# Optimization experiments

Hardware: AMD Instinct MI355X
Metric: run time of the kernel (lower is better)

## Reference

```python
import jax, jax.numpy as jnp
import numpy as np

N = 100000  # nodes (in_features)
D = 32      # out_features
E = 1600000 # edges


def setup_inputs() -> dict:
    key = jax.random.key(0)
    k1, k2, k3, k4, k5 = jax.random.split(key, 5)
    edge_row = jax.random.randint(k1, (E,), 0, N, dtype=jnp.int64)
    edge_col = jax.random.randint(k2, (E,), 0, N, dtype=jnp.int64)
    edge_val = jax.random.uniform(k3, (E,), dtype=jnp.float32)
    weight = jax.random.normal(k4, (N, D), dtype=jnp.float32)
    bias = jax.random.normal(k5, (D,), dtype=jnp.float32)
    return {"edge_row": edge_row, "edge_col": edge_col,
            "edge_val": edge_val, "weight": weight, "bias": bias}


def reference(edge_row, edge_col, edge_val, weight, bias):
    # out = adj @ weight + bias, adj given in COO form.
    # Gather weight rows per edge column, scale by edge value,
    # segment-sum into destination rows. [E, D] intermediate.
    contrib = edge_val[:, None] * jnp.take(weight, edge_col, axis=0)
    out = jax.ops.segment_sum(contrib, edge_row, num_segments=N)
    return out + bias
```

## Files before the change

kernel.cpp:

```cpp
#include <hip/hip_runtime.h>


#define FEAT 32
#define LOG_RPB 7
#define RPB (1 << LOG_RPB)
#define COLBITS 17
#define CMASK ((1u << COLBITS) - 1)
#define BMAX 1024
#define PCHUNK 4096
#define PTHREADS 1024
#define EPT (PCHUNK / PTHREADS)
#define CAPB 2560
#define CAP_MAX 32


__global__ __launch_bounds__(256) void gnn_zero(
    int* __restrict__ cursor, int* __restrict__ scnt, int B) {
    int i = blockIdx.x * 256 + threadIdx.x;
    if (i < B) cursor[i] = 0;
    if (i == B) *scnt = 0;
}

__global__ __launch_bounds__(PTHREADS) void gnn_part(
    const int* __restrict__ edge_row,
    const int* __restrict__ edge_col,
    const float* __restrict__ edge_val,
    int* __restrict__ cursor,
    float2* __restrict__ parts,
    float4* __restrict__ spill,
    int* __restrict__ scnt,
    int num_edges, int B) {
    __shared__ float2 lrec[PCHUNK];
    __shared__ unsigned short lbkt[PCHUNK];
    __shared__ int hcur[BMAX];
    __shared__ int st[BMAX];
    __shared__ int wtot[16], wbase[16];
    int t = threadIdx.x;
    hcur[t] = 0;
    __syncthreads();

    int e0 = blockIdx.x * PCHUNK;
    int cnt_chunk = num_edges - e0;
    if (cnt_chunk > PCHUNK) cnt_chunk = PCHUNK;

    int  r[EPT], c[EPT], bb[EPT], slot[EPT];
    float vv[EPT];
    int ebase = e0 + 4 * t;
    if (ebase + 3 < num_edges) {
        int4  r4 = *(const int4*)(edge_row + ebase);
        int4  c4 = *(const int4*)(edge_col + ebase);
        float4 v4 = *(const float4*)(edge_val + ebase);
        r[0] = r4.x; r[1] = r4.y; r[2] = r4.z; r[3] = r4.w;
        c[0] = c4.x; c[1] = c4.y; c[2] = c4.z; c[3] = c4.w;
        vv[0] = v4.x; vv[1] = v4.y; vv[2] = v4.z; vv[3] = v4.w;
    } else {
        #pragma unroll
        for (int k = 0; k < EPT; ++k) {
            int e = ebase + k;
            bool ok = e < num_edges;
            r[k]  = ok ? edge_row[e] : -1;
            c[k]  = ok ? edge_col[e] : 0;
            vv[k] = ok ? edge_val[e] : 0.f;
        }
    }
    #pragma unroll
    for (int k = 0; k < EPT; ++k) {
        if (r[k] >= 0) {
            bb[k] = r[k] >> LOG_RPB;
            slot[k] = atomicAdd(&hcur[bb[k]], 1);
        }
    }
    __syncthreads();

    int v = hcur[t];
    int wid = t >> 6, lane = t & 63;
    int x = v;
    #pragma unroll
    for (int off = 1; off < 64; off <<= 1) {
        int y = __shfl_up(x, off);
        if (lane >= off) x += y;
    }
    if (lane == 63) wtot[wid] = x;
    __syncthreads();
    if (t < 16) {
        int w = wtot[t], xx = w;
        #pragma unroll
        for (int off = 1; off < 16; off <<= 1) {
            int y = __shfl_up(xx, off);
            if (t >= off) xx += y;
        }
        wbase[t] = xx - w;
    }
    __syncthreads();
    int ex = x - v + wbase[wid];
    st[t] = ex;
    int rbase = 0;
    if (t < B && v) rbase = atomicAdd(&cursor[t], v);
    hcur[t] = rbase;
    __syncthreads();

    #pragma unroll
    for (int k = 0; k < EPT; ++k) {
        if (r[k] >= 0) {
            int pos = st[bb[k]] + slot[k];
            unsigned pk = (unsigned)c[k] |
                          ((unsigned)(r[k] & (RPB - 1)) << COLBITS);
            lrec[pos] = make_float2(__uint_as_float(pk), vv[k]);
            lbkt[pos] = (unsigned short)bb[k];
        }
    }
    __syncthreads();

    for (int i = t; i < cnt_chunk; i += PTHREADS) {
        int b2 = lbkt[i];
        float2 rec = lrec[i];
        int s = hcur[b2] + (i - st[b2]);
        if (s < CAPB) {
            parts[(long long)b2 * CAPB + s] = rec;
        } else {
            int si = atomicAdd(scnt, 1);
            unsigned pk = __float_as_uint(rec.x);
            spill[si] = make_float4(
                __uint_as_float((unsigned)(b2 << LOG_RPB) + (pk >> COLBITS)),
                __uint_as_float(pk & CMASK), rec.y, 0.f);
        }
    }
}

__global__ __launch_bounds__(512) void gnn_accum(
    const float2* __restrict__ parts,
    const int* __restrict__ cursor,
    const int* __restrict__ scnt,
    const float4* __restrict__ spill,
    const float* __restrict__ weight,
    const float* __restrict__ bias,
    float* __restrict__ out,
    int n_nodes) {
    __shared__ float2 srec[CAPB];
    __shared__ int h[RPB];
    __shared__ int rs[RPB + 1];
    int b = blockIdx.x, t = threadIdx.x;
    int n = cursor[b];
    int nspill = *scnt;
    int m = n < CAPB ? n : CAPB;
    const float2* p = parts + (long long)b * CAPB;

    float2 rec[CAPB / 512];
    int rl[CAPB / 512], slot[CAPB / 512];
    if (t < RPB) h[t] = 0;
    __syncthreads();
    #pragma unroll
    for (int k = 0; k < CAPB / 512; ++k) {
        int idx = t + k * 512;
        bool ok = idx < m;
        rec[k] = ok ? p[idx] : make_float2(0.f, 0.f);
        if (ok) {
            rl[k] = (int)((__float_as_uint(rec[k].x) >> COLBITS) & (RPB - 1));
            slot[k] = atomicAdd(&h[rl[k]], 1);
        }
    }
    __syncthreads();

    if (t < 64) {
        int a  = h[2 * t];
        int c2 = h[2 * t + 1];
        int pr = a + c2;
        int x = pr;
        #pragma unroll
        for (int off = 1; off < 64; off <<= 1) {
            int y = __shfl_up(x, off);
            if (t >= off) x += y;
        }
        int exc = x - pr;
        rs[2 * t] = exc;
        rs[2 * t + 1] = exc + a;
        if (t == 63) rs[RPB] = x;
    }
    __syncthreads();

    #pragma unroll
    for (int k = 0; k < CAPB / 512; ++k) {
        int idx = t + k * 512;
        if (idx < m) srec[rs[rl[k]] + slot[k]] = rec[k];
    }
    __syncthreads();

    int g = t >> 3;
    int l = t & 7;
    int row0 = b << LOG_RPB;
    float4 bf4 = ((const float4*)bias)[l];
    #pragma unroll 1
    for (int rr = 0; rr < 2; ++rr) {
        int rlc = (g << 1) + rr;
        int s = rs[rlc], e = rs[rlc + 1];
        float4 acc = make_float4(0.f, 0.f, 0.f, 0.f);
        for (int j = s; j < e; j += 8) {
            unsigned pk[8]; float vv[8];
            #pragma unroll
            for (int k = 0; k < 8; ++k) {
                int jj = j + k;
                float2 rc = srec[jj < e ? jj : s];
                pk[k] = __float_as_uint(rc.x);
                vv[k] = rc.y;
            }
            float4 w4[8];
            #pragma unroll
            for (int k = 0; k < 8; ++k)
                w4[k] = *(const float4*)(
                    weight + (long long)(pk[k] & CMASK) * FEAT + (l << 2));
            #pragma unroll
            for (int k = 0; k < 8; ++k) {
                float sc = (j + k < e) ? vv[k] : 0.f;
                acc.x += sc * w4[k].x;
                acc.y += sc * w4[k].y;
                acc.z += sc * w4[k].z;
                acc.w += sc * w4[k].w;
            }
        }
        if (nspill > 0) {
            for (int i = 0; i < nspill; ++i) {
                float4 sp = spill[i];
                if ((int)__float_as_uint(sp.x) == row0 + rlc) {
                    float4 wz = *(const float4*)(
                        weight + (long long)__float_as_uint(sp.y) * FEAT +
                        (l << 2));
                    acc.x += sp.z * wz.x;
                    acc.y += sp.z * wz.y;
                    acc.z += sp.z * wz.z;
                    acc.w += sp.z * wz.w;
                }
            }
        }
        int rrow = row0 + rlc;
        if (rrow < n_nodes) {
            float4 o = make_float4(acc.x + bf4.x, acc.y + bf4.y,
                                   acc.z + bf4.z, acc.w + bf4.w);
            *(float4*)(out + (long long)rrow * FEAT + (l << 2)) = o;
        }
    }
}


__global__ __launch_bounds__(256) void gnn_init(
    const float* __restrict__ bias, float* __restrict__ out,
    int* __restrict__ cnt, int total4, int n_nodes) {
    int i = blockIdx.x * blockDim.x + threadIdx.x;
    if (i < total4) {
        float4 bb = ((const float4*)bias)[i & 7];
        ((float4*)out)[i] = bb;
    }
    if (i < n_nodes) cnt[i] = 0;
}

__global__ __launch_bounds__(256) void gnn_bin(
    const int* __restrict__ edge_row,
    const int* __restrict__ edge_col,
    const float* __restrict__ edge_val,
    const float* __restrict__ weight,
    float2* __restrict__ bins,
    int* __restrict__ cnt,
    float* __restrict__ out,
    int num_edges, int cap) {
    int e = blockIdx.x * blockDim.x + threadIdx.x;
    if (e >= num_edges) return;
    int r = edge_row[e];
    int c = edge_col[e];
    float v = edge_val[e];
    int slot = atomicAdd(&cnt[r], 1);
    if (slot < cap) {
        bins[(long long)r * cap + slot] = make_float2(__int_as_float(c), v);
    } else {
        const float* w = weight + (long long)c * FEAT;
        #pragma unroll
        for (int f = 0; f < FEAT; ++f)
            atomicAdd(out + (long long)r * FEAT + f, v * w[f]);
    }
}

__global__ __launch_bounds__(256) void gnn_gather(
    const float2* __restrict__ bins,
    const int* __restrict__ cnt,
    const float* __restrict__ weight,
    float* __restrict__ out,
    int n_nodes, int cap) {
    int g = (blockIdx.x * blockDim.x + threadIdx.x) >> 5;
    int f = threadIdx.x & (FEAT - 1);
    if (g >= n_nodes) return;
    int n = cnt[g];
    n = n < cap ? n : cap;
    const float2* b = bins + (long long)g * cap;
    float a0 = 0.f, a1 = 0.f, a2 = 0.f, a3 = 0.f;
    int j = 0;
    for (; j + 4 <= n; j += 4) {
        float2 e0 = b[j], e1 = b[j + 1], e2 = b[j + 2], e3 = b[j + 3];
        a0 += e0.y * weight[(long long)__float_as_int(e0.x) * FEAT + f];
        a1 += e1.y * weight[(long long)__float_as_int(e1.x) * FEAT + f];
        a2 += e2.y * weight[(long long)__float_as_int(e2.x) * FEAT + f];
        a3 += e3.y * weight[(long long)__float_as_int(e3.x) * FEAT + f];
    }
    for (; j < n; ++j) {
        float2 e0 = b[j];
        a0 += e0.y * weight[(long long)__float_as_int(e0.x) * FEAT + f];
    }
    out[(long long)g * FEAT + f] += (a0 + a1) + (a2 + a3);
}


__global__ __launch_bounds__(256) void gnn_init_out(
    const float* __restrict__ bias, float* __restrict__ out, int total) {
    int i = blockIdx.x * blockDim.x + threadIdx.x;
    if (i < total) out[i] = bias[i & (FEAT - 1)];
}

__global__ __launch_bounds__(256) void gnn_scatter(
    const int* __restrict__ edge_row,
    const int* __restrict__ edge_col,
    const float* __restrict__ edge_val,
    const float* __restrict__ weight,
    float* __restrict__ out,
    int num_edges) {
    long long t = (long long)blockIdx.x * blockDim.x + threadIdx.x;
    int e = (int)(t >> 5);
    int f = (int)(t & (FEAT - 1));
    if (e < num_edges) {
        int r = edge_row[e];
        int c = edge_col[e];
        atomicAdd(out + r * FEAT + f, edge_val[e] * weight[c * FEAT + f]);
    }
}

extern "C" void kernel_launch(void* const* d_in, const int* in_sizes, int n_in,
                              void* d_out, int out_size, void* d_ws, size_t ws_size,
                              hipStream_t stream) {
    const int*   edge_row = (const int*)d_in[0];
    const int*   edge_col = (const int*)d_in[1];
    const float* edge_val = (const float*)d_in[2];
    const float* weight   = (const float*)d_in[3];
    const float* bias     = (const float*)d_in[4];
    float* out = (float*)d_out;

    const int E = in_sizes[0];
    const int total = out_size;
    const int N = total / FEAT;
    const int B = (N + RPB - 1) >> LOG_RPB;

    auto align256 = [](size_t x) { return (x + 255) & ~(size_t)255; };
    size_t cursor_off = 0;
    size_t scnt_off   = align256(cursor_off + (size_t)B * sizeof(int));
    size_t spill_off  = align256(scnt_off + sizeof(int));
    size_t parts_off  = align256(spill_off + (size_t)E * sizeof(float4));
    size_t need_v8    = parts_off + (size_t)B * CAPB * sizeof(float2);

    if (B >= 1 && B <= BMAX && N <= (1 << COLBITS) && E > 0 && ws_size >= need_v8) {
        int*    cursor = (int*)((char*)d_ws + cursor_off);
        int*    scnt   = (int*)((char*)d_ws + scnt_off);
        float4* spill  = (float4*)((char*)d_ws + spill_off);
        float2* parts  = (float2*)((char*)d_ws + parts_off);

        gnn_zero<<<(B + 1 + 255) / 256, 256, 0, stream>>>(cursor, scnt, B);
        gnn_part<<<(E + PCHUNK - 1) / PCHUNK, PTHREADS, 0, stream>>>(
            edge_row, edge_col, edge_val, cursor, parts, spill, scnt, E, B);
        gnn_accum<<<B, 512, 0, stream>>>(
            parts, cursor, scnt, spill, weight, bias, out, N);
        return;
    }

    size_t cnt_bytes = align256((size_t)N * sizeof(int));
    long long cap_ll = 0;
    if (ws_size > cnt_bytes)
        cap_ll = (long long)((ws_size - cnt_bytes) / ((size_t)N * sizeof(float2)));
    int cap = (int)(cap_ll > CAP_MAX ? CAP_MAX : cap_ll);

    if (cap >= 16) {
        int* cnt = (int*)d_ws;
        float2* bins = (float2*)((char*)d_ws + cnt_bytes);
        int total4 = total / 4;
        int init_threads = total4 > N ? total4 : N;
        gnn_init<<<(init_threads + 255) / 256, 256, 0, stream>>>(
            bias, out, cnt, total4, N);
        gnn_bin<<<(E + 255) / 256, 256, 0, stream>>>(
            edge_row, edge_col, edge_val, weight, bins, cnt, out, E, cap);
        long long gthreads = (long long)N * FEAT;
        gnn_gather<<<(int)((gthreads + 255) / 256), 256, 0, stream>>>(
            bins, cnt, weight, out, N, cap);
    } else {
        gnn_init_out<<<(total + 255) / 256, 256, 0, stream>>>(bias, out, total);
        long long threads = (long long)E * FEAT;
        gnn_scatter<<<(int)((threads + 255) / 256), 256, 0, stream>>>(
            edge_row, edge_col, edge_val, weight, out, E);
    }
}
```

Baseline: 122.1 us.

## Split accumulate kernel into per-bucket sort and wide per-row gather kernel

The fused accumulate kernel, one 512-thread block per 128-row bucket, is split in two. A sort kernel writes the row-sorted records and row offsets to global memory, and a new gather kernel uses 8 threads per row across many 256-thread blocks, sharing edge records through shuffles. The goal is more parallelism and occupancy for the latency-bound weight gathers, which previously ran on only about 782 blocks. The cost is an extra kernel launch, an extra global round trip for the sorted records, and a larger workspace requirement, which could make the fast path fall back if the workspace is too small.

```diff
diff --git a/kernel.cpp b/kernel.cpp
--- a/kernel.cpp
+++ b/kernel.cpp
@@ -127,21 +127,16 @@
     }
 }
 
-__global__ __launch_bounds__(512) void gnn_accum(
+__global__ __launch_bounds__(512) void gnn_sort(
     const float2* __restrict__ parts,
     const int* __restrict__ cursor,
-    const int* __restrict__ scnt,
-    const float4* __restrict__ spill,
-    const float* __restrict__ weight,
-    const float* __restrict__ bias,
-    float* __restrict__ out,
-    int n_nodes) {
+    float2* __restrict__ srec_g,
+    int* __restrict__ rs_g) {
     __shared__ float2 srec[CAPB];
     __shared__ int h[RPB];
     __shared__ int rs[RPB + 1];
     int b = blockIdx.x, t = threadIdx.x;
     int n = cursor[b];
-    int nspill = *scnt;
     int m = n < CAPB ? n : CAPB;
     const float2* p = parts + (long long)b * CAPB;
 
@@ -185,59 +180,89 @@
     }
     __syncthreads();
 
-    int g = t >> 3;
-    int l = t & 7;
-    int row0 = b << LOG_RPB;
+    for (int i = t; i < m; i += 512)
+        srec_g[(long long)b * CAPB + i] = srec[i];
+    if (t <= RPB)
+        rs_g[b * (RPB + 1) + t] = rs[t];
+}
+
+__global__ __launch_bounds__(256) void gnn_gather2(
+    const float2* __restrict__ srec_g,
+    const int* __restrict__ rs_g,
+    const int* __restrict__ scnt,
+    const float4* __restrict__ spill,
+    const float* __restrict__ weight,
+    const float* __restrict__ bias,
+    float* __restrict__ out,
+    int n_nodes) {
+    int gid = (blockIdx.x * 256 + threadIdx.x) >> 3;
+    if (gid >= n_nodes) return;
+    int l = threadIdx.x & 7;
+    int b  = gid >> LOG_RPB;
+    int rl = gid & (RPB - 1);
+    int cbase = b * (RPB + 1) + rl;
+    int s = rs_g[cbase], e = rs_g[cbase + 1];
+    const float2* p = srec_g + (long long)b * CAPB;
+    int gb = (threadIdx.x & 63) & ~7;
+
+    float4 acc = make_float4(0.f, 0.f, 0.f, 0.f);
+    int full = s + ((e - s) & ~7);
+    for (int j = s; j < full; j += 8) {
+        float2 my = p[j + l];
+        unsigned mpk = __float_as_uint(my.x);
+        float    mvv = my.y;
+        #pragma unroll
+        for (int k = 0; k < 8; ++k) {
+            unsigned pk = (unsigned)__shfl((int)mpk, gb + k);
+            float    vk = __shfl(mvv, gb + k);
+            const float4 w4 = *(const float4*)(
+                weight + (long long)(pk & CMASK) * FEAT + (l << 2));
+            acc.x += vk * w4.x;
+            acc.y += vk * w4.y;
+            acc.z += vk * w4.z;
+            acc.w += vk * w4.w;
+        }
+    }
+    if (full < e) {
+        int jj = full + l;
+        float2 my = p[jj < e ? jj : s];
+        unsigned mpk = __float_as_uint(my.x);
+        float    mvv = my.y;
+        int rem = e - full;
+        #pragma unroll
+        for (int k = 0; k < 8; ++k) {
+            if (k < rem) {
+                unsigned pk = (unsigned)__shfl((int)mpk, gb + k);
+                float    vk = __shfl(mvv, gb + k);
+                const float4 w4 = *(const float4*)(
+                    weight + (long long)(pk & CMASK) * FEAT + (l << 2));
+                acc.x += vk * w4.x;
+                acc.y += vk * w4.y;
+                acc.z += vk * w4.z;
+                acc.w += vk * w4.w;
+            }
+        }
+    }
+
+    int nspill = *scnt;
+    if (nspill > 0) {
+        for (int i = 0; i < nspill; ++i) {
+            float4 sp = spill[i];
+            if ((int)__float_as_uint(sp.x) == gid) {
+                const float4 wz = *(const float4*)(
+                    weight + (long long)__float_as_uint(sp.y) * FEAT + (l << 2));
+                acc.x += sp.z * wz.x;
+                acc.y += sp.z * wz.y;
+                acc.z += sp.z * wz.z;
+                acc.w += sp.z * wz.w;
+            }
+        }
+    }
+
     float4 bf4 = ((const float4*)bias)[l];
-    #pragma unroll 1
-    for (int rr = 0; rr < 2; ++rr) {
-        int rlc = (g << 1) + rr;
-        int s = rs[rlc], e = rs[rlc + 1];
-        float4 acc = make_float4(0.f, 0.f, 0.f, 0.f);
-        for (int j = s; j < e; j += 8) {
-            unsigned pk[8]; float vv[8];
-            #pragma unroll
-            for (int k = 0; k < 8; ++k) {
-                int jj = j + k;
-                float2 rc = srec[jj < e ? jj : s];
-                pk[k] = __float_as_uint(rc.x);
-                vv[k] = rc.y;
-            }
-            float4 w4[8];
-            #pragma unroll
-            for (int k = 0; k < 8; ++k)
-                w4[k] = *(const float4*)(
-                    weight + (long long)(pk[k] & CMASK) * FEAT + (l << 2));
-            #pragma unroll
-            for (int k = 0; k < 8; ++k) {
-                float sc = (j + k < e) ? vv[k] : 0.f;
-                acc.x += sc * w4[k].x;
-                acc.y += sc * w4[k].y;
-                acc.z += sc * w4[k].z;
-                acc.w += sc * w4[k].w;
-            }
-        }
-        if (nspill > 0) {
-            for (int i = 0; i < nspill; ++i) {
-                float4 sp = spill[i];
-                if ((int)__float_as_uint(sp.x) == row0 + rlc) {
-                    float4 wz = *(const float4*)(
-                        weight + (long long)__float_as_uint(sp.y) * FEAT +
-                        (l << 2));
-                    acc.x += sp.z * wz.x;
-                    acc.y += sp.z * wz.y;
-                    acc.z += sp.z * wz.z;
-                    acc.w += sp.z * wz.w;
-                }
-            }
-        }
-        int rrow = row0 + rlc;
-        if (rrow < n_nodes) {
-            float4 o = make_float4(acc.x + bf4.x, acc.y + bf4.y,
-                                   acc.z + bf4.z, acc.w + bf4.w);
-            *(float4*)(out + (long long)rrow * FEAT + (l << 2)) = o;
-        }
-    }
+    float4 o = make_float4(acc.x + bf4.x, acc.y + bf4.y,
+                           acc.z + bf4.z, acc.w + bf4.w);
+    *(float4*)(out + (long long)gid * FEAT + (l << 2)) = o;
 }
 
 
@@ -349,19 +374,25 @@
     size_t scnt_off   = align256(cursor_off + (size_t)B * sizeof(int));
     size_t spill_off  = align256(scnt_off + sizeof(int));
     size_t parts_off  = align256(spill_off + (size_t)E * sizeof(float4));
-    size_t need_v8    = parts_off + (size_t)B * CAPB * sizeof(float2);
-
-    if (B >= 1 && B <= BMAX && N <= (1 << COLBITS) && E > 0 && ws_size >= need_v8) {
+    size_t srec_off   = align256(parts_off + (size_t)B * CAPB * sizeof(float2));
+    size_t rs_off     = align256(srec_off + (size_t)B * CAPB * sizeof(float2));
+    size_t need_v9    = rs_off + (size_t)B * (RPB + 1) * sizeof(int);
+
+    if (B >= 1 && B <= BMAX && N <= (1 << COLBITS) && E > 0 && ws_size >= need_v9) {
         int*    cursor = (int*)((char*)d_ws + cursor_off);
         int*    scnt   = (int*)((char*)d_ws + scnt_off);
         float4* spill  = (float4*)((char*)d_ws + spill_off);
         float2* parts  = (float2*)((char*)d_ws + parts_off);
+        float2* srec_g = (float2*)((char*)d_ws + srec_off);
+        int*    rs_g   = (int*)((char*)d_ws + rs_off);
 
         gnn_zero<<<(B + 1 + 255) / 256, 256, 0, stream>>>(cursor, scnt, B);
         gnn_part<<<(E + PCHUNK - 1) / PCHUNK, PTHREADS, 0, stream>>>(
             edge_row, edge_col, edge_val, cursor, parts, spill, scnt, E, B);
-        gnn_accum<<<B, 512, 0, stream>>>(
-            parts, cursor, scnt, spill, weight, bias, out, N);
+        gnn_sort<<<B, 512, 0, stream>>>(parts, cursor, srec_g, rs_g);
+        long long gthreads = (long long)N * 8;
+        gnn_gather2<<<(int)((gthreads + 255) / 256), 256, 0, stream>>>(
+            srec_g, rs_g, scnt, spill, weight, bias, out, N);
         return;
     }
 
```

After: 131.7 us. +7.8%, slower.

## Split edge partitioning into coarse superblock pass and fine bucket pass

Applied to the files above, without the earlier changes.

Replaces the single-pass partition of edges into 782 fine row buckets with two passes. The first scatters into 49 superblocks of 2048 rows, and the second splits each superblock into 16 fine buckets of 128 rows. With far fewer destinations per chunk, each scatter writes larger contiguous runs, which should reduce uncoalesced global writes and per-bucket cursor atomics. The cost is an extra kernel launch and an additional read and write of all edge records through a new superblock buffer.

```diff
diff --git a/kernel.cpp b/kernel.cpp
--- a/kernel.cpp
+++ b/kernel.cpp
@@ -6,53 +6,57 @@
 #define RPB (1 << LOG_RPB)
 #define COLBITS 17
 #define CMASK ((1u << COLBITS) - 1)
+#define LOG_SBR 11
+#define SBROWS (1 << LOG_SBR)
+#define NSB_MAX 64
+#define SBCAP 36864
+#define BCHUNKS 9
+#define FPS (SBROWS / RPB)
 #define BMAX 1024
 #define PCHUNK 4096
 #define PTHREADS 1024
-#define EPT (PCHUNK / PTHREADS)
+#define EPT 4
 #define CAPB 2560
 #define CAP_MAX 32
 
 
-__global__ __launch_bounds__(256) void gnn_zero(
-    int* __restrict__ cursor, int* __restrict__ scnt, int B) {
+__global__ __launch_bounds__(256) void gnn_zero(int* __restrict__ p, int n) {
     int i = blockIdx.x * 256 + threadIdx.x;
-    if (i < B) cursor[i] = 0;
-    if (i == B) *scnt = 0;
-}
-
-__global__ __launch_bounds__(PTHREADS) void gnn_part(
+    if (i < n) p[i] = 0;
+}
+
+__global__ __launch_bounds__(PTHREADS) void gnn_parta(
     const int* __restrict__ edge_row,
     const int* __restrict__ edge_col,
     const float* __restrict__ edge_val,
-    int* __restrict__ cursor,
-    float2* __restrict__ parts,
+    int* __restrict__ cursor_sb,
+    float2* __restrict__ sbparts,
     float4* __restrict__ spill,
     int* __restrict__ scnt,
-    int num_edges, int B) {
+    int num_edges, int nsb) {
     __shared__ float2 lrec[PCHUNK];
-    __shared__ unsigned short lbkt[PCHUNK];
-    __shared__ int hcur[BMAX];
-    __shared__ int st[BMAX];
-    __shared__ int wtot[16], wbase[16];
+    __shared__ unsigned char lsb[PCHUNK];
+    __shared__ int hist[NSB_MAX];
+    __shared__ int st[NSB_MAX];
+    __shared__ int rb[NSB_MAX];
     int t = threadIdx.x;
-    hcur[t] = 0;
+    if (t < NSB_MAX) hist[t] = 0;
     __syncthreads();
 
     int e0 = blockIdx.x * PCHUNK;
     int cnt_chunk = num_edges - e0;
     if (cnt_chunk > PCHUNK) cnt_chunk = PCHUNK;
 
-    int  r[EPT], c[EPT], bb[EPT], slot[EPT];
+    int r[EPT], c[EPT], sb[EPT], slot[EPT];
     float vv[EPT];
     int ebase = e0 + 4 * t;
     if (ebase + 3 < num_edges) {
         int4  r4 = *(const int4*)(edge_row + ebase);
         int4  c4 = *(const int4*)(edge_col + ebase);
         float4 v4 = *(const float4*)(edge_val + ebase);
-        r[0] = r4.x; r[1] = r4.y; r[2] = r4.z; r[3] = r4.w;
-        c[0] = c4.x; c[1] = c4.y; c[2] = c4.z; c[3] = c4.w;
-        vv[0] = v4.x; vv[1] = v4.y; vv[2] = v4.z; vv[3] = v4.w;
+        r[0]=r4.x; r[1]=r4.y; r[2]=r4.z; r[3]=r4.w;
+        c[0]=c4.x; c[1]=c4.y; c[2]=c4.z; c[3]=c4.w;
+        vv[0]=v4.x; vv[1]=v4.y; vv[2]=v4.z; vv[3]=v4.w;
     } else {
         #pragma unroll
         for (int k = 0; k < EPT; ++k) {
@@ -66,70 +70,153 @@
     #pragma unroll
     for (int k = 0; k < EPT; ++k) {
         if (r[k] >= 0) {
-            bb[k] = r[k] >> LOG_RPB;
-            slot[k] = atomicAdd(&hcur[bb[k]], 1);
-        }
-    }
-    __syncthreads();
-
-    int v = hcur[t];
-    int wid = t >> 6, lane = t & 63;
-    int x = v;
-    #pragma unroll
-    for (int off = 1; off < 64; off <<= 1) {
-        int y = __shfl_up(x, off);
-        if (lane >= off) x += y;
-    }
-    if (lane == 63) wtot[wid] = x;
-    __syncthreads();
-    if (t < 16) {
-        int w = wtot[t], xx = w;
-        #pragma unroll
-        for (int off = 1; off < 16; off <<= 1) {
-            int y = __shfl_up(xx, off);
-            if (t >= off) xx += y;
-        }
-        wbase[t] = xx - w;
-    }
-    __syncthreads();
-    int ex = x - v + wbase[wid];
-    st[t] = ex;
-    int rbase = 0;
-    if (t < B && v) rbase = atomicAdd(&cursor[t], v);
-    hcur[t] = rbase;
+            sb[k] = r[k] >> LOG_SBR;
+            slot[k] = atomicAdd(&hist[sb[k]], 1);
+        }
+    }
+    __syncthreads();
+
+    if (t < NSB_MAX) {
+        int v = hist[t];
+        int x = v;
+        #pragma unroll
+        for (int off = 1; off < 64; off <<= 1) {
+            int y = __shfl_up(x, off);
+            if (t >= off) x += y;
+        }
+        st[t] = x - v;
+        rb[t] = (v && t < nsb) ? atomicAdd(&cursor_sb[t], v) : 0;
+    }
     __syncthreads();
 
     #pragma unroll
     for (int k = 0; k < EPT; ++k) {
         if (r[k] >= 0) {
-            int pos = st[bb[k]] + slot[k];
+            int pos = st[sb[k]] + slot[k];
             unsigned pk = (unsigned)c[k] |
-                          ((unsigned)(r[k] & (RPB - 1)) << COLBITS);
+                          ((unsigned)(r[k] & (SBROWS - 1)) << COLBITS);
             lrec[pos] = make_float2(__uint_as_float(pk), vv[k]);
-            lbkt[pos] = (unsigned short)bb[k];
+            lsb[pos] = (unsigned char)sb[k];
         }
     }
     __syncthreads();
 
     for (int i = t; i < cnt_chunk; i += PTHREADS) {
-        int b2 = lbkt[i];
+        int b2 = lsb[i];
         float2 rec = lrec[i];
-        int s = hcur[b2] + (i - st[b2]);
-        if (s < CAPB) {
-            parts[(long long)b2 * CAPB + s] = rec;
+        int s = rb[b2] + (i - st[b2]);
+        if (s < SBCAP) {
+            sbparts[(long long)b2 * SBCAP + s] = rec;
         } else {
             int si = atomicAdd(scnt, 1);
             unsigned pk = __float_as_uint(rec.x);
             spill[si] = make_float4(
-                __uint_as_float((unsigned)(b2 << LOG_RPB) + (pk >> COLBITS)),
+                __uint_as_float((unsigned)(b2 << LOG_SBR) + (pk >> COLBITS)),
                 __uint_as_float(pk & CMASK), rec.y, 0.f);
+        }
+    }
+}
+
+__global__ __launch_bounds__(PTHREADS) void gnn_partb(
+    const float2* __restrict__ sbparts,
+    const int* __restrict__ cursor_sb,
+    int* __restrict__ cursor_fine,
+    float2* __restrict__ parts,
+    float4* __restrict__ spill,
+    int* __restrict__ scnt,
+    int n_fine) {
+    __shared__ float2 lrec[PCHUNK];
+    __shared__ unsigned char lfb[PCHUNK];
+    __shared__ int hist[FPS];
+    __shared__ int st[FPS];
+    __shared__ int rb[FPS];
+    int t = threadIdx.x;
+    int sb = blockIdx.x / BCHUNKS;
+    int ch = blockIdx.x % BCHUNKS;
+    int n_sb = cursor_sb[sb];
+    if (n_sb > SBCAP) n_sb = SBCAP;
+    int lo = ch * PCHUNK;
+    int m = n_sb - lo;
+    if (m <= 0) return;
+    if (m > PCHUNK) m = PCHUNK;
+    if (t < FPS) hist[t] = 0;
+    __syncthreads();
+
+    const float2* src = sbparts + (long long)sb * SBCAP + lo;
+
+    float2 rec[EPT];
+    int fb[EPT], slot[EPT];
+    int rbase = 4 * t;
+    if (rbase + 3 < m) {
+        float4 q0 = *(const float4*)(src + rbase);
+        float4 q1 = *(const float4*)(src + rbase + 2);
+        rec[0] = make_float2(q0.x, q0.y);
+        rec[1] = make_float2(q0.z, q0.w);
+        rec[2] = make_float2(q1.x, q1.y);
+        rec[3] = make_float2(q1.z, q1.w);
+    } else {
+        #pragma unroll
+        for (int k = 0; k < EPT; ++k) {
+            int idx = rbase + k;
+            rec[k] = (idx < m) ? src[idx] : make_float2(__uint_as_float(~0u), 0.f);
+        }
+    }
+    #pragma unroll
+    for (int k = 0; k < EPT; ++k) {
+        unsigned pk = __float_as_uint(rec[k].x);
+        if (pk != ~0u) {
+            fb[k] = (int)((pk >> COLBITS) >> LOG_RPB);
+            slot[k] = atomicAdd(&hist[fb[k]], 1);
+        } else fb[k] = -1;
+    }
+    __syncthreads();
+
+    if (t < FPS) {
+        int v = hist[t];
+        int x = v;
+        #pragma unroll
+        for (int off = 1; off < FPS; off <<= 1) {
+            int y = __shfl_up(x, off);
+            if (t >= off) x += y;
+        }
+        st[t] = x - v;
+        int fg = sb * FPS + t;
+        rb[t] = (v && fg < n_fine) ? atomicAdd(&cursor_fine[fg], v) : 0;
+    }
+    __syncthreads();
+
+    #pragma unroll
+    for (int k = 0; k < EPT; ++k) {
+        if (fb[k] >= 0) {
+            int pos = st[fb[k]] + slot[k];
+            unsigned pk = __float_as_uint(rec[k].x);
+            unsigned npk = pk & ((1u << (COLBITS + LOG_RPB)) - 1);
+            lrec[pos] = make_float2(__uint_as_float(npk), rec[k].y);
+            lfb[pos] = (unsigned char)fb[k];
+        }
+    }
+    __syncthreads();
+
+    for (int i = t; i < m; i += PTHREADS) {
+        int f2 = lfb[i];
+        float2 rc = lrec[i];
+        int fg = sb * FPS + f2;
+        int s = rb[f2] + (i - st[f2]);
+        if (s < CAPB) {
+            parts[(long long)fg * CAPB + s] = rc;
+        } else {
+            int si = atomicAdd(scnt, 1);
+            unsigned pk = __float_as_uint(rc.x);
+            spill[si] = make_float4(
+                __uint_as_float((unsigned)(fg << LOG_RPB) + (pk >> COLBITS)),
+                __uint_as_float(pk & CMASK), rc.y, 0.f);
         }
     }
 }
 
 __global__ __launch_bounds__(512) void gnn_accum(
     const float2* __restrict__ parts,
-    const int* __restrict__ cursor,
+    const int* __restrict__ cursor_fine,
     const int* __restrict__ scnt,
     const float4* __restrict__ spill,
     const float* __restrict__ weight,
@@ -140,7 +227,7 @@
     __shared__ int h[RPB];
     __shared__ int rs[RPB + 1];
     int b = blockIdx.x, t = threadIdx.x;
-    int n = cursor[b];
+    int n = cursor_fine[b];
     int nspill = *scnt;
     int m = n < CAPB ? n : CAPB;
     const float2* p = parts + (long long)b * CAPB;
@@ -195,13 +282,13 @@
         int s = rs[rlc], e = rs[rlc + 1];
         float4 acc = make_float4(0.f, 0.f, 0.f, 0.f);
         for (int j = s; j < e; j += 8) {
-            unsigned pk[8]; float vv[8];
+            unsigned pk[8]; float vvv[8];
             #pragma unroll
             for (int k = 0; k < 8; ++k) {
                 int jj = j + k;
                 float2 rc = srec[jj < e ? jj : s];
                 pk[k] = __float_as_uint(rc.x);
-                vv[k] = rc.y;
+                vvv[k] = rc.y;
             }
             float4 w4[8];
             #pragma unroll
@@ -210,7 +297,7 @@
                     weight + (long long)(pk[k] & CMASK) * FEAT + (l << 2));
             #pragma unroll
             for (int k = 0; k < 8; ++k) {
-                float sc = (j + k < e) ? vv[k] : 0.f;
+                float sc = (j + k < e) ? vvv[k] : 0.f;
                 acc.x += sc * w4[k].x;
                 acc.y += sc * w4[k].y;
                 acc.z += sc * w4[k].z;
@@ -221,7 +308,7 @@
             for (int i = 0; i < nspill; ++i) {
                 float4 sp = spill[i];
                 if ((int)__float_as_uint(sp.x) == row0 + rlc) {
-                    float4 wz = *(const float4*)(
+                    const float4 wz = *(const float4*)(
                         weight + (long long)__float_as_uint(sp.y) * FEAT +
                         (l << 2));
                     acc.x += sp.z * wz.x;
@@ -343,25 +430,34 @@
     const int total = out_size;
     const int N = total / FEAT;
     const int B = (N + RPB - 1) >> LOG_RPB;
+    const int NSB = (N + SBROWS - 1) >> LOG_SBR;
 
     auto align256 = [](size_t x) { return (x + 255) & ~(size_t)255; };
-    size_t cursor_off = 0;
-    size_t scnt_off   = align256(cursor_off + (size_t)B * sizeof(int));
-    size_t spill_off  = align256(scnt_off + sizeof(int));
-    size_t parts_off  = align256(spill_off + (size_t)E * sizeof(float4));
-    size_t need_v8    = parts_off + (size_t)B * CAPB * sizeof(float2);
-
-    if (B >= 1 && B <= BMAX && N <= (1 << COLBITS) && E > 0 && ws_size >= need_v8) {
-        int*    cursor = (int*)((char*)d_ws + cursor_off);
-        int*    scnt   = (int*)((char*)d_ws + scnt_off);
-        float4* spill  = (float4*)((char*)d_ws + spill_off);
-        float2* parts  = (float2*)((char*)d_ws + parts_off);
-
-        gnn_zero<<<(B + 1 + 255) / 256, 256, 0, stream>>>(cursor, scnt, B);
-        gnn_part<<<(E + PCHUNK - 1) / PCHUNK, PTHREADS, 0, stream>>>(
-            edge_row, edge_col, edge_val, cursor, parts, spill, scnt, E, B);
+    size_t ints = (size_t)NSB + (size_t)B + 1;
+    size_t spill_off   = align256(ints * sizeof(int));
+    size_t sbparts_off = align256(spill_off + (size_t)E * sizeof(float4));
+    size_t parts_off   = align256(sbparts_off +
+                                  (size_t)NSB * SBCAP * sizeof(float2));
+    size_t need_v11    = parts_off + (size_t)B * CAPB * sizeof(float2);
+
+    if (NSB >= 1 && NSB <= NSB_MAX && B <= BMAX && N <= (1 << COLBITS) &&
+        E > 0 && ws_size >= need_v11) {
+        int*    cursor_sb   = (int*)d_ws;
+        int*    cursor_fine = cursor_sb + NSB;
+        int*    scnt        = cursor_fine + B;
+        float4* spill       = (float4*)((char*)d_ws + spill_off);
+        float2* sbparts     = (float2*)((char*)d_ws + sbparts_off);
+        float2* parts       = (float2*)((char*)d_ws + parts_off);
+
+        gnn_zero<<<(int)((ints + 255) / 256), 256, 0, stream>>>(
+            cursor_sb, (int)ints);
+        gnn_parta<<<(E + PCHUNK - 1) / PCHUNK, PTHREADS, 0, stream>>>(
+            edge_row, edge_col, edge_val, cursor_sb, sbparts, spill, scnt,
+            E, NSB);
+        gnn_partb<<<NSB * BCHUNKS, PTHREADS, 0, stream>>>(
+            sbparts, cursor_sb, cursor_fine, parts, spill, scnt, B);
         gnn_accum<<<B, 512, 0, stream>>>(
-            parts, cursor, scnt, spill, weight, bias, out, N);
+            parts, cursor_fine, scnt, spill, weight, bias, out, N);
         return;
     }
 
```

After: 126.3 us. 1.03x slower.

## Split accumulation into four column zones with partial buffers and a reduce kernel

Applied to the files above, without the earlier changes.

The accumulate kernel launches four blocks per row bucket instead of one. Each block keeps only the edges whose column falls in its quarter of the node range, so there are more blocks in flight and each block gathers from a smaller slice of the weight matrix. Each block writes its own partial row sums, and a new reduce kernel adds the four partials, applies any spilled edges, and adds the bias. The price is that every bucket's edge list is read four times, a partial buffer four times the size of the output is written and read back, and the gather inner loop unroll drops from 8 to 4.

```diff
diff --git a/kernel.cpp b/kernel.cpp
--- a/kernel.cpp
+++ b/kernel.cpp
@@ -11,6 +11,7 @@
 #define PTHREADS 1024
 #define EPT (PCHUNK / PTHREADS)
 #define CAPB 2560
+#define CAPZ 1024
 #define CAP_MAX 32
 
 
@@ -50,9 +51,9 @@
         int4  r4 = *(const int4*)(edge_row + ebase);
         int4  c4 = *(const int4*)(edge_col + ebase);
         float4 v4 = *(const float4*)(edge_val + ebase);
-        r[0] = r4.x; r[1] = r4.y; r[2] = r4.z; r[3] = r4.w;
-        c[0] = c4.x; c[1] = c4.y; c[2] = c4.z; c[3] = c4.w;
-        vv[0] = v4.x; vv[1] = v4.y; vv[2] = v4.z; vv[3] = v4.w;
+        r[0]=r4.x; r[1]=r4.y; r[2]=r4.z; r[3]=r4.w;
+        c[0]=c4.x; c[1]=c4.y; c[2]=c4.z; c[3]=c4.w;
+        vv[0]=v4.x; vv[1]=v4.y; vv[2]=v4.z; vv[3]=v4.w;
     } else {
         #pragma unroll
         for (int k = 0; k < EPT; ++k) {
@@ -127,26 +128,28 @@
     }
 }
 
-__global__ __launch_bounds__(512) void gnn_accum(
+__global__ __launch_bounds__(512) void gnn_accum_z(
     const float2* __restrict__ parts,
     const int* __restrict__ cursor,
-    const int* __restrict__ scnt,
-    const float4* __restrict__ spill,
     const float* __restrict__ weight,
-    const float* __restrict__ bias,
-    float* __restrict__ out,
-    int n_nodes) {
-    __shared__ float2 srec[CAPB];
+    float* __restrict__ partial,
+    float4* __restrict__ spill,
+    int* __restrict__ scnt,
+    int n_nodes, int z1, int z2, int z3) {
+    __shared__ float2 srec[CAPZ];
     __shared__ int h[RPB];
     __shared__ int rs[RPB + 1];
-    int b = blockIdx.x, t = threadIdx.x;
+    int bid = blockIdx.x, t = threadIdx.x;
+    int zone = bid & 3;
+    int b = bid >> 2;
     int n = cursor[b];
-    int nspill = *scnt;
     int m = n < CAPB ? n : CAPB;
     const float2* p = parts + (long long)b * CAPB;
+    int row0 = b << LOG_RPB;
 
     float2 rec[CAPB / 512];
     int rl[CAPB / 512], slot[CAPB / 512];
+    bool keep[CAPB / 512];
     if (t < RPB) h[t] = 0;
     __syncthreads();
     #pragma unroll
@@ -154,8 +157,12 @@
         int idx = t + k * 512;
         bool ok = idx < m;
         rec[k] = ok ? p[idx] : make_float2(0.f, 0.f);
-        if (ok) {
-            rl[k] = (int)((__float_as_uint(rec[k].x) >> COLBITS) & (RPB - 1));
+        unsigned pk = __float_as_uint(rec[k].x);
+        int c = (int)(pk & CMASK);
+        int zz = (c >= z1) + (c >= z2) + (c >= z3);
+        keep[k] = ok && (zz == zone);
+        if (keep[k]) {
+            rl[k] = (int)((pk >> COLBITS) & (RPB - 1));
             slot[k] = atomicAdd(&h[rl[k]], 1);
         }
     }
@@ -180,64 +187,95 @@
 
     #pragma unroll
     for (int k = 0; k < CAPB / 512; ++k) {
-        int idx = t + k * 512;
-        if (idx < m) srec[rs[rl[k]] + slot[k]] = rec[k];
+        if (keep[k]) {
+            int pos = rs[rl[k]] + slot[k];
+            if (pos < CAPZ) {
+                srec[pos] = rec[k];
+            } else {
+                int si = atomicAdd(scnt, 1);
+                unsigned pk = __float_as_uint(rec[k].x);
+                spill[si] = make_float4(
+                    __uint_as_float((unsigned)(row0 + rl[k])),
+                    __uint_as_float(pk & CMASK), rec[k].y, 0.f);
+            }
+        }
     }
     __syncthreads();
 
     int g = t >> 3;
     int l = t & 7;
-    int row0 = b << LOG_RPB;
-    float4 bf4 = ((const float4*)bias)[l];
     #pragma unroll 1
     for (int rr = 0; rr < 2; ++rr) {
         int rlc = (g << 1) + rr;
         int s = rs[rlc], e = rs[rlc + 1];
+        if (s > CAPZ) s = CAPZ;
+        if (e > CAPZ) e = CAPZ;
         float4 acc = make_float4(0.f, 0.f, 0.f, 0.f);
-        for (int j = s; j < e; j += 8) {
-            unsigned pk[8]; float vv[8];
+        for (int j = s; j < e; j += 4) {
+            unsigned pk[4]; float vvv[4];
             #pragma unroll
-            for (int k = 0; k < 8; ++k) {
+            for (int k = 0; k < 4; ++k) {
                 int jj = j + k;
                 float2 rc = srec[jj < e ? jj : s];
                 pk[k] = __float_as_uint(rc.x);
-                vv[k] = rc.y;
+                vvv[k] = rc.y;
             }
-            float4 w4[8];
+            float4 w4[4];
             #pragma unroll
-            for (int k = 0; k < 8; ++k)
+            for (int k = 0; k < 4; ++k)
                 w4[k] = *(const float4*)(
                     weight + (long long)(pk[k] & CMASK) * FEAT + (l << 2));
             #pragma unroll
-            for (int k = 0; k < 8; ++k) {
-                float sc = (j + k < e) ? vv[k] : 0.f;
+            for (int k = 0; k < 4; ++k) {
+                float sc = (j + k < e) ? vvv[k] : 0.f;
                 acc.x += sc * w4[k].x;
                 acc.y += sc * w4[k].y;
                 acc.z += sc * w4[k].z;
                 acc.w += sc * w4[k].w;
             }
         }
-        if (nspill > 0) {
-            for (int i = 0; i < nspill; ++i) {
-                float4 sp = spill[i];
-                if ((int)__float_as_uint(sp.x) == row0 + rlc) {
-                    float4 wz = *(const float4*)(
-                        weight + (long long)__float_as_uint(sp.y) * FEAT +
-                        (l << 2));
-                    acc.x += sp.z * wz.x;
-                    acc.y += sp.z * wz.y;
-                    acc.z += sp.z * wz.z;
-                    acc.w += sp.z * wz.w;
-                }
+        int rrow = row0 + rlc;
+        if (rrow < n_nodes)
+            *(float4*)(partial + ((long long)zone * n_nodes + rrow) * FEAT +
+                       (l << 2)) = acc;
+    }
+}
+
+__global__ __launch_bounds__(256) void gnn_reduce(
+    const float* __restrict__ partial,
+    const int* __restrict__ scnt,
+    const float4* __restrict__ spill,
+    const float* __restrict__ weight,
+    const float* __restrict__ bias,
+    float* __restrict__ out,
+    int n_nodes) {
+    int gid = (blockIdx.x * 256 + threadIdx.x) >> 3;
+    if (gid >= n_nodes) return;
+    int l = threadIdx.x & 7;
+    float4 a = make_float4(0.f, 0.f, 0.f, 0.f);
+    #pragma unroll
+    for (int z = 0; z < 4; ++z) {
+        float4 q = *(const float4*)(
+            partial + ((long long)z * n_nodes + gid) * FEAT + (l << 2));
+        a.x += q.x; a.y += q.y; a.z += q.z; a.w += q.w;
+    }
+    int ns = *scnt;
+    if (ns > 0) {
+        for (int i = 0; i < ns; ++i) {
+            float4 sp = spill[i];
+            if ((int)__float_as_uint(sp.x) == gid) {
+                const float4 wz = *(const float4*)(
+                    weight + (long long)__float_as_uint(sp.y) * FEAT + (l << 2));
+                a.x += sp.z * wz.x;
+                a.y += sp.z * wz.y;
+                a.z += sp.z * wz.z;
+                a.w += sp.z * wz.w;
             }
         }
-        int rrow = row0 + rlc;
-        if (rrow < n_nodes) {
-            float4 o = make_float4(acc.x + bf4.x, acc.y + bf4.y,
-                                   acc.z + bf4.z, acc.w + bf4.w);
-            *(float4*)(out + (long long)rrow * FEAT + (l << 2)) = o;
-        }
-    }
+    }
+    float4 bf4 = ((const float4*)bias)[l];
+    float4 o = make_float4(a.x + bf4.x, a.y + bf4.y, a.z + bf4.z, a.w + bf4.w);
+    *(float4*)(out + (long long)gid * FEAT + (l << 2)) = o;
 }
 
 
@@ -345,23 +383,32 @@
     const int B = (N + RPB - 1) >> LOG_RPB;
 
     auto align256 = [](size_t x) { return (x + 255) & ~(size_t)255; };
-    size_t cursor_off = 0;
-    size_t scnt_off   = align256(cursor_off + (size_t)B * sizeof(int));
-    size_t spill_off  = align256(scnt_off + sizeof(int));
-    size_t parts_off  = align256(spill_off + (size_t)E * sizeof(float4));
-    size_t need_v8    = parts_off + (size_t)B * CAPB * sizeof(float2);
-
-    if (B >= 1 && B <= BMAX && N <= (1 << COLBITS) && E > 0 && ws_size >= need_v8) {
-        int*    cursor = (int*)((char*)d_ws + cursor_off);
-        int*    scnt   = (int*)((char*)d_ws + scnt_off);
-        float4* spill  = (float4*)((char*)d_ws + spill_off);
-        float2* parts  = (float2*)((char*)d_ws + parts_off);
+    size_t cursor_off  = 0;
+    size_t scnt_off    = align256(cursor_off + (size_t)B * sizeof(int));
+    size_t spill_off   = align256(scnt_off + sizeof(int));
+    size_t parts_off   = align256(spill_off + (size_t)E * sizeof(float4));
+    size_t partial_off = align256(parts_off + (size_t)B * CAPB * sizeof(float2));
+    size_t need_v12    = partial_off + 4ull * N * FEAT * sizeof(float);
+
+    if (B >= 1 && B <= BMAX && N <= (1 << COLBITS) && E > 0 &&
+        ws_size >= need_v12) {
+        int*    cursor  = (int*)((char*)d_ws + cursor_off);
+        int*    scnt    = (int*)((char*)d_ws + scnt_off);
+        float4* spill   = (float4*)((char*)d_ws + spill_off);
+        float2* parts   = (float2*)((char*)d_ws + parts_off);
+        float*  partial = (float*)((char*)d_ws + partial_off);
+
+        int zdiv = (N + 3) / 4;
+        int z1 = zdiv, z2 = 2 * zdiv, z3 = 3 * zdiv;
 
         gnn_zero<<<(B + 1 + 255) / 256, 256, 0, stream>>>(cursor, scnt, B);
         gnn_part<<<(E + PCHUNK - 1) / PCHUNK, PTHREADS, 0, stream>>>(
             edge_row, edge_col, edge_val, cursor, parts, spill, scnt, E, B);
-        gnn_accum<<<B, 512, 0, stream>>>(
-            parts, cursor, scnt, spill, weight, bias, out, N);
+        gnn_accum_z<<<B * 4, 512, 0, stream>>>(
+            parts, cursor, weight, partial, spill, scnt, N, z1, z2, z3);
+        long long rthreads = (long long)N * 8;
+        gnn_reduce<<<(int)((rthreads + 255) / 256), 256, 0, stream>>>(
+            partial, scnt, spill, weight, bias, out, N);
         return;
     }
 
```

Result: slower. 131.9 us (+8.0%).
